# Optimization experiments

Measured on AMD Instinct MI355X. Metric: run time of the kernel, lower is better.

The kernel has to match this reference:

```python
import jax, jax.numpy as jnp
import numpy as np

TRANSLATION_SCALE = 1.0
ROTATION_SCALE = 0.1
EPS = 1e-05


def setup_inputs() -> dict:
    key = jax.random.key(0)
    uv = jax.random.normal(key, (2000000, 3), dtype=jnp.float32)
    return {"uv": uv}


def reference(uv):
    # uv: [B, 3] = [x, y, p_yaw]
    B = uv.shape[0]
    w = uv[:, 2] * ROTATION_SCALE                     # omega_z, [B]
    theta_sqr = w * w
    theta = jnp.sqrt(theta_sqr)                       # = |w|
    A = jnp.sin(theta) / (theta + EPS)                # sin(theta)/theta
    Bc = (1.0 - jnp.cos(theta)) / (theta_sqr + EPS)   # (1-cos)/theta^2
    C = (1.0 - A) / (theta_sqr + EPS)                 # (1-A)/theta^2

    # skew(w) for z-only rotation: [[0,-w,0],[w,0,0],[0,0,0]]
    zeros = jnp.zeros_like(w)
    skew = jnp.stack([
        jnp.stack([zeros, -w, zeros], axis=-1),
        jnp.stack([w, zeros, zeros], axis=-1),
        jnp.stack([zeros, zeros, zeros], axis=-1),
    ], axis=-2)                                        # [B,3,3]
    # skew @ skew = diag(-w^2, -w^2, 0)
    skew2 = jnp.stack([
        jnp.stack([-theta_sqr, zeros, zeros], axis=-1),
        jnp.stack([zeros, -theta_sqr, zeros], axis=-1),
        jnp.stack([zeros, zeros, zeros], axis=-1),
    ], axis=-2)                                        # [B,3,3]

    I3 = jnp.eye(3, dtype=uv.dtype)
    R = I3 + A[:, None, None] * skew + Bc[:, None, None] * skew2   # rotation [B,3,3]
    V = I3 + Bc[:, None, None] * skew + C[:, None, None] * skew2   # left-Jacobian-like [B,3,3]

    u = jnp.stack([uv[:, 0] * TRANSLATION_SCALE,
                   uv[:, 1] * TRANSLATION_SCALE,
                   zeros], axis=-1)                    # [B,3]
    t = jnp.einsum('bij,bj->bi', V, u)                 # translation [B,3]

    top = jnp.concatenate([R, t[:, :, None]], axis=-1) # [B,3,4]
    bottom = jnp.broadcast_to(jnp.array([0., 0., 0., 1.], dtype=uv.dtype), (B, 1, 4))
    return jnp.concatenate([top, bottom], axis=-2)     # [B,4,4]
```

## Files before the change

### kernel.cpp

```cpp
#include <hip/hip_runtime.h>


#define ROTATION_SCALE 0.1f
#define EPS_F 1e-5f

__global__ __launch_bounds__(256) void lie_se3_kernel(
    const float* __restrict__ uv, float4* __restrict__ out, int B) {
  int t = blockIdx.x * blockDim.x + threadIdx.x;
  int row = t >> 2;
  int part = t & 3;
  if (row >= B) return;

  float x = uv[3 * row + 0];
  float y = uv[3 * row + 1];
  float p = uv[3 * row + 2];

  float w = p * ROTATION_SCALE;
  float ts = w * w;
  float th = fabsf(w);
  float s = __sinf(th);
  float c = __cosf(th);
  float A  = s / (th + EPS_F);
  float Bc = (1.0f - c) / (ts + EPS_F);
  float C  = (1.0f - A) / (ts + EPS_F);

  float R00 = 1.0f - Bc * ts;
  float Aw  = A * w;
  float V00 = 1.0f - C * ts;
  float Bw  = Bc * w;
  float t0 = V00 * x - Bw * y;
  float t1 = Bw * x + V00 * y;

  float4 v;
  v.x = (part == 0) ? R00 : ((part == 1) ? Aw : 0.0f);
  v.y = (part == 0) ? -Aw : ((part == 1) ? R00 : 0.0f);
  v.z = (part == 2) ? 1.0f : 0.0f;
  v.w = (part == 0) ? t0 : ((part == 1) ? t1 : ((part == 3) ? 1.0f : 0.0f));

  out[t] = v;
}

extern "C" void kernel_launch(void* const* d_in, const int* in_sizes, int n_in,
                              void* d_out, int out_size, void* d_ws, size_t ws_size,
                              hipStream_t stream) {
  const float* uv = (const float*)d_in[0];
  float4* out = (float4*)d_out;
  int B = in_sizes[0] / 3;
  long long threads = 4LL * B;
  int block = 256;
  int grid = (int)((threads + block - 1) / block);
  lie_se3_kernel<<<grid, block, 0, stream>>>(uv, out, B);
}
```

Measured before the change: 149.7 us.

## Compute one row per thread and stage 4x4 output through shared memory

Each thread now handles one input row instead of four threads redundantly reloading and recomputing the same row. It writes all four float4 rows of the matrix to LDS, syncs, then the block stores them with coalesced float4 writes. This cuts redundant loads and transcendental math by a factor of four, at the cost of an LDS round trip, a barrier, and 16KB of shared memory per block.

Measured after the change: 140.3 us. -6.3%, faster.

```diff
diff --git a/kernel.cpp b/kernel.cpp
--- a/kernel.cpp
+++ b/kernel.cpp
@@ -6,14 +6,17 @@
 
 __global__ __launch_bounds__(256) void lie_se3_kernel(
     const float* __restrict__ uv, float4* __restrict__ out, int B) {
-  int t = blockIdx.x * blockDim.x + threadIdx.x;
-  int row = t >> 2;
-  int part = t & 3;
-  if (row >= B) return;
+  __shared__ float4 smem[1024];
 
-  float x = uv[3 * row + 0];
-  float y = uv[3 * row + 1];
-  float p = uv[3 * row + 2];
+  int tid = threadIdx.x;
+  int m = blockIdx.x * 256 + tid;
+
+  float x = 0.0f, y = 0.0f, p = 0.0f;
+  if (m < B) {
+    x = uv[3 * m + 0];
+    y = uv[3 * m + 1];
+    p = uv[3 * m + 2];
+  }
 
   float w = p * ROTATION_SCALE;
   float ts = w * w;
@@ -31,13 +34,20 @@
   float t0 = V00 * x - Bw * y;
   float t1 = Bw * x + V00 * y;
 
-  float4 v;
-  v.x = (part == 0) ? R00 : ((part == 1) ? Aw : 0.0f);
-  v.y = (part == 0) ? -Aw : ((part == 1) ? R00 : 0.0f);
-  v.z = (part == 2) ? 1.0f : 0.0f;
-  v.w = (part == 0) ? t0 : ((part == 1) ? t1 : ((part == 3) ? 1.0f : 0.0f));
+  smem[4 * tid + 0] = make_float4(R00, -Aw, 0.0f, t0);
+  smem[4 * tid + 1] = make_float4(Aw, R00, 0.0f, t1);
+  smem[4 * tid + 2] = make_float4(0.0f, 0.0f, 1.0f, 0.0f);
+  smem[4 * tid + 3] = make_float4(0.0f, 0.0f, 0.0f, 1.0f);
+  __syncthreads();
 
-  out[t] = v;
+  long long base = (long long)blockIdx.x * 1024;
+  long long limit = 4LL * B;
+  #pragma unroll
+  for (int k = 0; k < 4; ++k) {
+    int idx = tid + k * 256;
+    long long g = base + idx;
+    if (g < limit) out[g] = smem[idx];
+  }
 }
 
 extern "C" void kernel_launch(void* const* d_in, const int* in_sizes, int n_in,
@@ -46,8 +56,7 @@
   const float* uv = (const float*)d_in[0];
   float4* out = (float4*)d_out;
   int B = in_sizes[0] / 3;
-  long long threads = 4LL * B;
   int block = 256;
-  int grid = (int)((threads + block - 1) / block);
+  int grid = (B + block - 1) / block;
   lie_se3_kernel<<<grid, block, 0, stream>>>(uv, out, B);
 }
```
